# Optimization experiments

Hardware: AMD Instinct MI355X
Metric: run time of the kernel (lower is better)

Reference implementation:

```python
import jax, jax.numpy as jnp
import numpy as np

N_NODES = 50000
N_EDGES = 800000
IN_F, HID_F, OUT_F = 96, 96, 32


def setup_inputs() -> dict:
    key = jax.random.key(0)
    k1, k2, k3, k4, k5 = jax.random.split(key, 5)
    x = jax.random.normal(k1, (N_NODES, IN_F), dtype=jnp.float32)
    src = jax.random.randint(k2, (N_EDGES,), 0, N_NODES, dtype=jnp.int32)
    dst = jax.random.randint(k3, (N_EDGES,), 0, N_NODES, dtype=jnp.int32)
    W1 = jax.random.normal(k4, (IN_F, HID_F), dtype=jnp.float32) / np.sqrt(IN_F)
    b1 = jnp.zeros((HID_F,), dtype=jnp.float32)
    W2 = jax.random.normal(k5, (HID_F, OUT_F), dtype=jnp.float32) / np.sqrt(HID_F)
    b2 = jnp.zeros((OUT_F,), dtype=jnp.float32)
    return {"x": x, "src": src, "dst": dst, "W1": W1, "b1": b1, "W2": W2, "b2": b2}


def _graph_conv(src, dst, n_nodes, h, W, b):
    # DGL GraphConv, norm='both': D_out^{-1/2} A D_in^{-1/2} h W + b
    ones = jnp.ones((src.shape[0],), dtype=h.dtype)
    deg_out = jax.ops.segment_sum(ones, src, num_segments=n_nodes)  # src out-degree
    deg_in = jax.ops.segment_sum(ones, dst, num_segments=n_nodes)   # dst in-degree
    norm_src = jax.lax.rsqrt(jnp.maximum(deg_out, 1.0))
    norm_dst = jax.lax.rsqrt(jnp.maximum(deg_in, 1.0))
    h = h * norm_src[:, None]
    msg = h[src]                                                    # [E, F] gather
    agg = jax.ops.segment_sum(msg, dst, num_segments=n_nodes)       # [N, F] scatter-add
    agg = agg * norm_dst[:, None]
    return agg @ W + b


def reference(x, src, dst, W1, b1, W2, b2):
    n = x.shape[0]
    h = _graph_conv(src, dst, n, x, W1, b1)
    h = jax.nn.relu(h)
    h = _graph_conv(src, dst, n, h, W2, b2)
    return h
```

## Files before the change

kernel.cpp:

```cpp
#include <hip/hip_runtime.h>


constexpr int NN = 50000;
constexpr int NE = 800000;
constexpr int CAP = 64;
constexpr int HNODES = 16384;
constexpr int HWORDS = 8192;
constexpr int NCH = 4;
constexpr int NSL = 64;
constexpr int NNP = 50048;
constexpr int PREF_NB = (NN + 255) / 256;
constexpr int CVTW_NB = 48;
constexpr int FILL_NB = NCH * NSL;
constexpr int CVTX_NB = ((NN + 1) * 12 + 255) / 256;

using bf16x8 = __attribute__((ext_vector_type(8))) short;
using u16x8  = __attribute__((ext_vector_type(8))) unsigned short;
using f32x4  = __attribute__((ext_vector_type(4))) float;

__device__ __forceinline__ ushort f2b(float f) {
    unsigned u = __float_as_uint(f);
    u += 0x7FFFu + ((u >> 16) & 1u);
    return (ushort)(u >> 16);
}
__device__ __forceinline__ float b2f(ushort h) {
    return __uint_as_float(((unsigned)h) << 16);
}

__global__ void hist_kernel(const int* __restrict__ src, const int* __restrict__ dst,
                            ushort* __restrict__ pS, ushort* __restrict__ pD, int ne) {
    __shared__ int bins[HWORDS];
    const int ch = blockIdx.x, sl = blockIdx.y;
    const int lo = ch * HNODES;
    for (int i = threadIdx.x; i < HWORDS; i += 256) bins[i] = 0;
    __syncthreads();
    const int per4 = (ne / NSL) / 4;
    const int i0 = sl * per4;
    const int4* src4 = (const int4*)src;
    const int4* dst4 = (const int4*)dst;
    for (int i = i0 + threadIdx.x; i < i0 + per4; i += 256) {
        int4 s = src4[i];
        int4 d = dst4[i];
        unsigned u;
        u = (unsigned)(s.x - lo); if (u < HNODES) atomicAdd(bins + (u >> 1), 1 << ((u & 1) * 16));
        u = (unsigned)(s.y - lo); if (u < HNODES) atomicAdd(bins + (u >> 1), 1 << ((u & 1) * 16));
        u = (unsigned)(s.z - lo); if (u < HNODES) atomicAdd(bins + (u >> 1), 1 << ((u & 1) * 16));
        u = (unsigned)(s.w - lo); if (u < HNODES) atomicAdd(bins + (u >> 1), 1 << ((u & 1) * 16));
        u = (unsigned)(d.x - lo); if (u < HNODES) atomicAdd(bins + (u >> 1), 1 << ((u & 1) * 16 + 8));
        u = (unsigned)(d.y - lo); if (u < HNODES) atomicAdd(bins + (u >> 1), 1 << ((u & 1) * 16 + 8));
        u = (unsigned)(d.z - lo); if (u < HNODES) atomicAdd(bins + (u >> 1), 1 << ((u & 1) * 16 + 8));
        u = (unsigned)(d.w - lo); if (u < HNODES) atomicAdd(bins + (u >> 1), 1 << ((u & 1) * 16 + 8));
    }
    __syncthreads();
    for (int pi = threadIdx.x; pi < HWORDS; pi += 256) {
        int node = lo + 2 * pi;
        if (node >= NN) break;
        int w = bins[pi];
        unsigned sE = w & 0xFF, dE = (w >> 8) & 0xFF, sO = (w >> 16) & 0xFF, dO = (w >> 24) & 0xFF;
        if (node + 1 < NN) {
            *(unsigned*)&pS[(size_t)sl * NNP + node] = sE | (sO << 16);
            *(unsigned*)&pD[(size_t)sl * NNP + node] = dE | (dO << 16);
        } else {
            pS[(size_t)sl * NNP + node] = (ushort)sE;
            pD[(size_t)sl * NNP + node] = (ushort)dE;
        }
    }
}

__global__ void prefix_cvtw_kernel(const ushort* __restrict__ pS, ushort* __restrict__ pD,
                                   float* __restrict__ ns, int* __restrict__ cnt,
                                   const float* __restrict__ W1, const float* __restrict__ W2,
                                   ushort* __restrict__ W1t, ushort* __restrict__ W2t, int n) {
    int b = blockIdx.x;
    if (b < PREF_NB) {
        int i = b * 256 + threadIdx.x;
        if (i >= n) return;
        int sS = 0, run = 0;
#pragma unroll
        for (int sl = 0; sl < NSL; ++sl) {
            sS += pS[(size_t)sl * NNP + i];
            int c = pD[(size_t)sl * NNP + i];
            pD[(size_t)sl * NNP + i] = (ushort)run;
            run += c;
        }
        ns[i] = rsqrtf(fmaxf((float)sS, 1.0f));
        cnt[i] = run;
    } else {
        int i = (b - PREF_NB) * 256 + threadIdx.x;
        if (i < 96 * 96) {
            int k = i / 96, c = i % 96;
            W1t[c * 96 + k] = f2b(W1[i]);
        } else {
            int j = i - 96 * 96;
            int k = j / 32, c = j % 32;
            W2t[c * 96 + k] = f2b(W2[j]);
        }
    }
}

__global__ void fill_cvtx_kernel(const int* __restrict__ src, const int* __restrict__ dst,
                                 const ushort* __restrict__ pD, ushort* __restrict__ slots,
                                 const float* __restrict__ x, const float* __restrict__ ns,
                                 ushort* __restrict__ xh, int ne, int n) {
    __shared__ int cur[HWORDS];
    int b = blockIdx.x;
    if (b < FILL_NB) {
        const int ch = b / NSL, sl = b % NSL;
        const int lo = ch * HNODES;
        for (int pi = threadIdx.x; pi < HWORDS; pi += 256) {
            int node = lo + 2 * pi;
            int lov = (node < NN) ? (int)pD[(size_t)sl * NNP + node] : 0;
            int hiv = (node + 1 < NN) ? (int)pD[(size_t)sl * NNP + node + 1] : 0;
            cur[pi] = lov | (hiv << 16);
        }
        __syncthreads();
        const int per4 = (ne / NSL) / 4;
        const int i0 = sl * per4;
        const int4* src4 = (const int4*)src;
        const int4* dst4 = (const int4*)dst;
        for (int i = i0 + threadIdx.x; i < i0 + per4; i += 256) {
            int4 d = dst4[i];
            int4 s = src4[i];
            unsigned u; int sh, old, p;
            u = (unsigned)(d.x - lo);
            if (u < HNODES) { sh = (u & 1) * 16; old = atomicAdd(cur + (u >> 1), 1 << sh);
                p = (old >> sh) & 0xFFFF; if (p < CAP) slots[((size_t)(lo + u) << 6) + p] = (ushort)s.x; }
            u = (unsigned)(d.y - lo);
            if (u < HNODES) { sh = (u & 1) * 16; old = atomicAdd(cur + (u >> 1), 1 << sh);
                p = (old >> sh) & 0xFFFF; if (p < CAP) slots[((size_t)(lo + u) << 6) + p] = (ushort)s.y; }
            u = (unsigned)(d.z - lo);
            if (u < HNODES) { sh = (u & 1) * 16; old = atomicAdd(cur + (u >> 1), 1 << sh);
                p = (old >> sh) & 0xFFFF; if (p < CAP) slots[((size_t)(lo + u) << 6) + p] = (ushort)s.z; }
            u = (unsigned)(d.w - lo);
            if (u < HNODES) { sh = (u & 1) * 16; old = atomicAdd(cur + (u >> 1), 1 << sh);
                p = (old >> sh) & 0xFFFF; if (p < CAP) slots[((size_t)(lo + u) << 6) + p] = (ushort)s.w; }
        }
    } else {
        int t = (b - FILL_NB) * 256 + threadIdx.x;
        if (t >= (n + 1) * 12) return;
        int r = t / 12;
        u16x8 o;
        if (r == n) {
#pragma unroll
            for (int u = 0; u < 8; ++u) o[u] = 0;
        } else {
            float s = ns[r];
            const float4* p = (const float4*)(x) + (size_t)t * 2;
            float4 v0 = p[0], v1 = p[1];
            o[0] = f2b(s * v0.x); o[1] = f2b(s * v0.y); o[2] = f2b(s * v0.z); o[3] = f2b(s * v0.w);
            o[4] = f2b(s * v1.x); o[5] = f2b(s * v1.y); o[6] = f2b(s * v1.z); o[7] = f2b(s * v1.w);
        }
        *(u16x8*)&xh[(size_t)t * 8] = o;
    }
}

__global__ void agg1_kernel(const ushort* __restrict__ xh, const int* __restrict__ cnt,
                            const ushort* __restrict__ slots, ushort* __restrict__ AB, int n) {
    int tid = blockIdx.x * 256 + threadIdx.x;
    int r = tid / 12, q = tid % 12;
    if (r >= n) return;
    int deg = min(cnt[r], CAP);
    const ushort* br = slots + ((size_t)r << 6);
    float acc[8] = {};
    for (int j0 = 0; j0 < deg; j0 += 8) {
        u16x8 sl8 = *(const u16x8*)(br + j0);
        int s0 = (j0 + 0 < deg) ? (int)sl8[0] : n;
        int s1 = (j0 + 1 < deg) ? (int)sl8[1] : n;
        int s2 = (j0 + 2 < deg) ? (int)sl8[2] : n;
        int s3 = (j0 + 3 < deg) ? (int)sl8[3] : n;
        int s4 = (j0 + 4 < deg) ? (int)sl8[4] : n;
        int s5 = (j0 + 5 < deg) ? (int)sl8[5] : n;
        int s6 = (j0 + 6 < deg) ? (int)sl8[6] : n;
        int s7 = (j0 + 7 < deg) ? (int)sl8[7] : n;
        u16x8 v0 = *(const u16x8*)&xh[(size_t)s0 * 96 + q * 8];
        u16x8 v1 = *(const u16x8*)&xh[(size_t)s1 * 96 + q * 8];
        u16x8 v2 = *(const u16x8*)&xh[(size_t)s2 * 96 + q * 8];
        u16x8 v3 = *(const u16x8*)&xh[(size_t)s3 * 96 + q * 8];
        u16x8 v4 = *(const u16x8*)&xh[(size_t)s4 * 96 + q * 8];
        u16x8 v5 = *(const u16x8*)&xh[(size_t)s5 * 96 + q * 8];
        u16x8 v6 = *(const u16x8*)&xh[(size_t)s6 * 96 + q * 8];
        u16x8 v7 = *(const u16x8*)&xh[(size_t)s7 * 96 + q * 8];
#pragma unroll
        for (int t = 0; t < 8; ++t) acc[t] += b2f(v0[t]);
#pragma unroll
        for (int t = 0; t < 8; ++t) acc[t] += b2f(v1[t]);
#pragma unroll
        for (int t = 0; t < 8; ++t) acc[t] += b2f(v2[t]);
#pragma unroll
        for (int t = 0; t < 8; ++t) acc[t] += b2f(v3[t]);
#pragma unroll
        for (int t = 0; t < 8; ++t) acc[t] += b2f(v4[t]);
#pragma unroll
        for (int t = 0; t < 8; ++t) acc[t] += b2f(v5[t]);
#pragma unroll
        for (int t = 0; t < 8; ++t) acc[t] += b2f(v6[t]);
#pragma unroll
        for (int t = 0; t < 8; ++t) acc[t] += b2f(v7[t]);
    }
    u16x8 o;
#pragma unroll
    for (int t = 0; t < 8; ++t) o[t] = f2b(acc[t]);
    *(u16x8*)&AB[(size_t)r * 96 + q * 8] = o;
}

__global__ void __launch_bounds__(256) gemm12_fused(
        const ushort* __restrict__ AB, const ushort* __restrict__ W1t,
        const ushort* __restrict__ W2t, const float* __restrict__ b1,
        const float* __restrict__ ns, const int* __restrict__ cnt,
        ushort* __restrict__ t2h, int n) {
    __shared__ ushort Wl1[96 * 104];
    __shared__ ushort Wl2[32 * 104];
    __shared__ ushort Hl[64 * 104];
    for (int i = threadIdx.x; i < 1152; i += 256) {
        int nr = i / 12, k = (i % 12) * 8;
        *(bf16x8*)&Wl1[nr * 104 + k] = *(const bf16x8*)&W1t[nr * 96 + k];
    }
    for (int i = threadIdx.x; i < 384; i += 256) {
        int nr = i / 12, k = (i % 12) * 8;
        *(bf16x8*)&Wl2[nr * 104 + k] = *(const bf16x8*)&W2t[nr * 96 + k];
    }
    __syncthreads();

    const int lane = threadIdx.x & 63;
    const int w = threadIdx.x >> 6;
    const int rl = lane & 15, kg = lane >> 4;
    const int rowbase = blockIdx.x * 64 + w * 16;

    const ushort* arow = AB + (size_t)(rowbase + rl) * 96 + kg * 8;
    bf16x8 a0 = *(const bf16x8*)(arow);
    bf16x8 a1 = *(const bf16x8*)(arow + 32);
    bf16x8 a2 = *(const bf16x8*)(arow + 64);
    f32x4 acc1[6] = {};
#pragma unroll
    for (int nt = 0; nt < 6; ++nt) {
        const ushort* wr = &Wl1[(nt * 16 + rl) * 104 + kg * 8];
        acc1[nt] = __builtin_amdgcn_mfma_f32_16x16x32_bf16(a0, *(const bf16x8*)(wr),      acc1[nt], 0, 0, 0);
        acc1[nt] = __builtin_amdgcn_mfma_f32_16x16x32_bf16(a1, *(const bf16x8*)(wr + 32), acc1[nt], 0, 0, 0);
        acc1[nt] = __builtin_amdgcn_mfma_f32_16x16x32_bf16(a2, *(const bf16x8*)(wr + 64), acc1[nt], 0, 0, 0);
    }
    const int r0 = rowbase + kg * 4;
    float sj[4];
#pragma unroll
    for (int j = 0; j < 4; ++j) sj[j] = rsqrtf(fmaxf((float)cnt[r0 + j], 1.0f));
#pragma unroll
    for (int nt = 0; nt < 6; ++nt) {
        int col = nt * 16 + rl;
        float bc = b1[col];
#pragma unroll
        for (int j = 0; j < 4; ++j)
            Hl[(w * 16 + kg * 4 + j) * 104 + col] = f2b(fmaxf(acc1[nt][j] * sj[j] + bc, 0.f));
    }
    __syncthreads();

    const ushort* hrow = &Hl[(w * 16 + rl) * 104 + kg * 8];
    bf16x8 h0 = *(const bf16x8*)(hrow);
    bf16x8 h1 = *(const bf16x8*)(hrow + 32);
    bf16x8 h2 = *(const bf16x8*)(hrow + 64);
    f32x4 acc2[2] = {};
#pragma unroll
    for (int nt = 0; nt < 2; ++nt) {
        const ushort* wr = &Wl2[(nt * 16 + rl) * 104 + kg * 8];
        acc2[nt] = __builtin_amdgcn_mfma_f32_16x16x32_bf16(h0, *(const bf16x8*)(wr),      acc2[nt], 0, 0, 0);
        acc2[nt] = __builtin_amdgcn_mfma_f32_16x16x32_bf16(h1, *(const bf16x8*)(wr + 32), acc2[nt], 0, 0, 0);
        acc2[nt] = __builtin_amdgcn_mfma_f32_16x16x32_bf16(h2, *(const bf16x8*)(wr + 64), acc2[nt], 0, 0, 0);
    }
    float sn[4];
#pragma unroll
    for (int j = 0; j < 4; ++j) sn[j] = ns[r0 + j];
#pragma unroll
    for (int nt = 0; nt < 2; ++nt) {
        int col = nt * 16 + rl;
#pragma unroll
        for (int j = 0; j < 4; ++j) {
            float val = (r0 + j < n) ? acc2[nt][j] * sn[j] : 0.f;
            t2h[(size_t)(r0 + j) * 32 + col] = f2b(val);
        }
    }
}

__global__ void agg2_kernel(const ushort* __restrict__ t2h, const float* __restrict__ b2,
                            const int* __restrict__ cnt, const ushort* __restrict__ slots,
                            float* __restrict__ out, int n) {
    int tid = blockIdx.x * 256 + threadIdx.x;
    int r = tid / 4, q = tid % 4;
    if (r >= n) return;
    int deg = min(cnt[r], CAP);
    const ushort* br = slots + ((size_t)r << 6);
    float acc[8] = {};
    for (int j0 = 0; j0 < deg; j0 += 8) {
        u16x8 sl8 = *(const u16x8*)(br + j0);
        int s0 = (j0 + 0 < deg) ? (int)sl8[0] : n;
        int s1 = (j0 + 1 < deg) ? (int)sl8[1] : n;
        int s2 = (j0 + 2 < deg) ? (int)sl8[2] : n;
        int s3 = (j0 + 3 < deg) ? (int)sl8[3] : n;
        int s4 = (j0 + 4 < deg) ? (int)sl8[4] : n;
        int s5 = (j0 + 5 < deg) ? (int)sl8[5] : n;
        int s6 = (j0 + 6 < deg) ? (int)sl8[6] : n;
        int s7 = (j0 + 7 < deg) ? (int)sl8[7] : n;
        u16x8 v0 = *(const u16x8*)&t2h[(size_t)s0 * 32 + q * 8];
        u16x8 v1 = *(const u16x8*)&t2h[(size_t)s1 * 32 + q * 8];
        u16x8 v2 = *(const u16x8*)&t2h[(size_t)s2 * 32 + q * 8];
        u16x8 v3 = *(const u16x8*)&t2h[(size_t)s3 * 32 + q * 8];
        u16x8 v4 = *(const u16x8*)&t2h[(size_t)s4 * 32 + q * 8];
        u16x8 v5 = *(const u16x8*)&t2h[(size_t)s5 * 32 + q * 8];
        u16x8 v6 = *(const u16x8*)&t2h[(size_t)s6 * 32 + q * 8];
        u16x8 v7 = *(const u16x8*)&t2h[(size_t)s7 * 32 + q * 8];
#pragma unroll
        for (int t = 0; t < 8; ++t) acc[t] += b2f(v0[t]);
#pragma unroll
        for (int t = 0; t < 8; ++t) acc[t] += b2f(v1[t]);
#pragma unroll
        for (int t = 0; t < 8; ++t) acc[t] += b2f(v2[t]);
#pragma unroll
        for (int t = 0; t < 8; ++t) acc[t] += b2f(v3[t]);
#pragma unroll
        for (int t = 0; t < 8; ++t) acc[t] += b2f(v4[t]);
#pragma unroll
        for (int t = 0; t < 8; ++t) acc[t] += b2f(v5[t]);
#pragma unroll
        for (int t = 0; t < 8; ++t) acc[t] += b2f(v6[t]);
#pragma unroll
        for (int t = 0; t < 8; ++t) acc[t] += b2f(v7[t]);
    }
    float sd = rsqrtf(fmaxf((float)deg, 1.0f));
    const float4* bb = (const float4*)(b2 + q * 8);
    float4 bv0 = bb[0], bv1 = bb[1];
    float4 o0, o1;
    o0.x = acc[0] * sd + bv0.x; o0.y = acc[1] * sd + bv0.y;
    o0.z = acc[2] * sd + bv0.z; o0.w = acc[3] * sd + bv0.w;
    o1.x = acc[4] * sd + bv1.x; o1.y = acc[5] * sd + bv1.y;
    o1.z = acc[6] * sd + bv1.z; o1.w = acc[7] * sd + bv1.w;
    float4* po = (float4*)&out[(size_t)r * 32 + q * 8];
    po[0] = o0; po[1] = o1;
}

extern "C" void kernel_launch(void* const* d_in, const int* in_sizes, int n_in,
                              void* d_out, int out_size, void* d_ws, size_t ws_size,
                              hipStream_t stream) {
    const float* x   = (const float*)d_in[0];
    const int*   src = (const int*)d_in[1];
    const int*   dst = (const int*)d_in[2];
    const float* W1  = (const float*)d_in[3];
    const float* b1  = (const float*)d_in[4];
    const float* W2  = (const float*)d_in[5];
    const float* b2  = (const float*)d_in[6];
    float* out = (float*)d_out;

    int*    cnt   = (int*)d_ws;
    float*  ns    = (float*)(cnt + NNP);
    ushort* slots = (ushort*)(ns + NNP);
    ushort* pS    = slots + (size_t)NN * CAP;
    ushort* pD    = pS + (size_t)NSL * NNP;
    ushort* xh    = pD + (size_t)NSL * NNP;
    ushort* AB    = xh + (size_t)NNP * 96;
    ushort* t2h   = AB + (size_t)NNP * 96;
    ushort* W1t   = t2h + (size_t)NNP * 32;
    ushort* W2t   = W1t + 96 * 96;

    hist_kernel<<<dim3(NCH, NSL), 256, 0, stream>>>(src, dst, pS, pD, NE);
    prefix_cvtw_kernel<<<PREF_NB + CVTW_NB, 256, 0, stream>>>(pS, pD, ns, cnt, W1, W2, W1t, W2t, NN);
    fill_cvtx_kernel<<<FILL_NB + CVTX_NB, 256, 0, stream>>>(src, dst, pD, slots, x, ns, xh, NE, NN);

    agg1_kernel<<<(NN * 12 + 255) / 256, 256, 0, stream>>>(xh, cnt, slots, AB, NN);
    gemm12_fused<<<NNP / 64, 256, 0, stream>>>(AB, W1t, W2t, b1, ns, cnt, t2h, NN);
    agg2_kernel<<<(NN * 4 + 255) / 256, 256, 0, stream>>>(t2h, b2, cnt, slots, out, NN);
}
```

Baseline: 92.70 us.

## Pack degree histograms as 8-bit counters and halve node chunks

Per-slice degree histograms and prefix offsets now use one byte per node, four nodes per shared-memory word, instead of 16-bit fields. This lets each block cover about 25k nodes, so the number of node chunks drops from four to two. As a result each edge slice is read half as often in the histogram and fill kernels, and the pS/pD arrays shrink by half. The trade-off is more shared memory per histogram block, which may lower occupancy, and it relies on per-slice counts and per-node in-degree prefixes fitting in 8 bits.

```diff
diff --git a/kernel.cpp b/kernel.cpp
--- a/kernel.cpp
+++ b/kernel.cpp
@@ -4,11 +4,11 @@
 constexpr int NN = 50000;
 constexpr int NE = 800000;
 constexpr int CAP = 64;
-constexpr int HNODES = 16384;
-constexpr int HWORDS = 8192;
-constexpr int NCH = 4;
+constexpr int NNP = 50048;
+constexpr int HN  = 25024;
+constexpr int HW  = HN / 4;
+constexpr int NCH = 2;
 constexpr int NSL = 64;
-constexpr int NNP = 50048;
 constexpr int PREF_NB = (NN + 255) / 256;
 constexpr int CVTW_NB = 48;
 constexpr int FILL_NB = NCH * NSL;
@@ -28,11 +28,13 @@
 }
 
 __global__ void hist_kernel(const int* __restrict__ src, const int* __restrict__ dst,
-                            ushort* __restrict__ pS, ushort* __restrict__ pD, int ne) {
-    __shared__ int bins[HWORDS];
+                            unsigned char* __restrict__ pS, unsigned char* __restrict__ pD,
+                            int ne) {
+    __shared__ int binsS[HW];
+    __shared__ int binsD[HW];
     const int ch = blockIdx.x, sl = blockIdx.y;
-    const int lo = ch * HNODES;
-    for (int i = threadIdx.x; i < HWORDS; i += 256) bins[i] = 0;
+    const int lo = ch * HN;
+    for (int i = threadIdx.x; i < HW; i += 256) { binsS[i] = 0; binsD[i] = 0; }
     __syncthreads();
     const int per4 = (ne / NSL) / 4;
     const int i0 = sl * per4;
@@ -42,32 +44,26 @@
         int4 s = src4[i];
         int4 d = dst4[i];
         unsigned u;
-        u = (unsigned)(s.x - lo); if (u < HNODES) atomicAdd(bins + (u >> 1), 1 << ((u & 1) * 16));
-        u = (unsigned)(s.y - lo); if (u < HNODES) atomicAdd(bins + (u >> 1), 1 << ((u & 1) * 16));
-        u = (unsigned)(s.z - lo); if (u < HNODES) atomicAdd(bins + (u >> 1), 1 << ((u & 1) * 16));
-        u = (unsigned)(s.w - lo); if (u < HNODES) atomicAdd(bins + (u >> 1), 1 << ((u & 1) * 16));
-        u = (unsigned)(d.x - lo); if (u < HNODES) atomicAdd(bins + (u >> 1), 1 << ((u & 1) * 16 + 8));
-        u = (unsigned)(d.y - lo); if (u < HNODES) atomicAdd(bins + (u >> 1), 1 << ((u & 1) * 16 + 8));
-        u = (unsigned)(d.z - lo); if (u < HNODES) atomicAdd(bins + (u >> 1), 1 << ((u & 1) * 16 + 8));
-        u = (unsigned)(d.w - lo); if (u < HNODES) atomicAdd(bins + (u >> 1), 1 << ((u & 1) * 16 + 8));
+        u = (unsigned)(s.x - lo); if (u < HN) atomicAdd(binsS + (u >> 2), 1 << ((u & 3) * 8));
+        u = (unsigned)(s.y - lo); if (u < HN) atomicAdd(binsS + (u >> 2), 1 << ((u & 3) * 8));
+        u = (unsigned)(s.z - lo); if (u < HN) atomicAdd(binsS + (u >> 2), 1 << ((u & 3) * 8));
+        u = (unsigned)(s.w - lo); if (u < HN) atomicAdd(binsS + (u >> 2), 1 << ((u & 3) * 8));
+        u = (unsigned)(d.x - lo); if (u < HN) atomicAdd(binsD + (u >> 2), 1 << ((u & 3) * 8));
+        u = (unsigned)(d.y - lo); if (u < HN) atomicAdd(binsD + (u >> 2), 1 << ((u & 3) * 8));
+        u = (unsigned)(d.z - lo); if (u < HN) atomicAdd(binsD + (u >> 2), 1 << ((u & 3) * 8));
+        u = (unsigned)(d.w - lo); if (u < HN) atomicAdd(binsD + (u >> 2), 1 << ((u & 3) * 8));
     }
     __syncthreads();
-    for (int pi = threadIdx.x; pi < HWORDS; pi += 256) {
-        int node = lo + 2 * pi;
-        if (node >= NN) break;
-        int w = bins[pi];
-        unsigned sE = w & 0xFF, dE = (w >> 8) & 0xFF, sO = (w >> 16) & 0xFF, dO = (w >> 24) & 0xFF;
-        if (node + 1 < NN) {
-            *(unsigned*)&pS[(size_t)sl * NNP + node] = sE | (sO << 16);
-            *(unsigned*)&pD[(size_t)sl * NNP + node] = dE | (dO << 16);
-        } else {
-            pS[(size_t)sl * NNP + node] = (ushort)sE;
-            pD[(size_t)sl * NNP + node] = (ushort)dE;
-        }
-    }
-}
-
-__global__ void prefix_cvtw_kernel(const ushort* __restrict__ pS, ushort* __restrict__ pD,
+    int* oS = (int*)(pS + (size_t)sl * NNP + lo);
+    int* oD = (int*)(pD + (size_t)sl * NNP + lo);
+    for (int t = threadIdx.x; t < HW; t += 256) {
+        oS[t] = binsS[t];
+        oD[t] = binsD[t];
+    }
+}
+
+__global__ void prefix_cvtw_kernel(const unsigned char* __restrict__ pS,
+                                   unsigned char* __restrict__ pD,
                                    float* __restrict__ ns, int* __restrict__ cnt,
                                    const float* __restrict__ W1, const float* __restrict__ W2,
                                    ushort* __restrict__ W1t, ushort* __restrict__ W2t, int n) {
@@ -80,7 +76,7 @@
         for (int sl = 0; sl < NSL; ++sl) {
             sS += pS[(size_t)sl * NNP + i];
             int c = pD[(size_t)sl * NNP + i];
-            pD[(size_t)sl * NNP + i] = (ushort)run;
+            pD[(size_t)sl * NNP + i] = (unsigned char)run;
             run += c;
         }
         ns[i] = rsqrtf(fmaxf((float)sS, 1.0f));
@@ -99,20 +95,17 @@
 }
 
 __global__ void fill_cvtx_kernel(const int* __restrict__ src, const int* __restrict__ dst,
-                                 const ushort* __restrict__ pD, ushort* __restrict__ slots,
+                                 const unsigned char* __restrict__ pD,
+                                 ushort* __restrict__ slots,
                                  const float* __restrict__ x, const float* __restrict__ ns,
                                  ushort* __restrict__ xh, int ne, int n) {
-    __shared__ int cur[HWORDS];
+    __shared__ int cur[HW];
     int b = blockIdx.x;
     if (b < FILL_NB) {
-        const int ch = b / NSL, sl = b % NSL;
-        const int lo = ch * HNODES;
-        for (int pi = threadIdx.x; pi < HWORDS; pi += 256) {
-            int node = lo + 2 * pi;
-            int lov = (node < NN) ? (int)pD[(size_t)sl * NNP + node] : 0;
-            int hiv = (node + 1 < NN) ? (int)pD[(size_t)sl * NNP + node + 1] : 0;
-            cur[pi] = lov | (hiv << 16);
-        }
+        const int ch = b >> 6, sl = b & 63;
+        const int lo = ch * HN;
+        const int* ip = (const int*)(pD + (size_t)sl * NNP + lo);
+        for (int t = threadIdx.x; t < HW; t += 256) cur[t] = ip[t];
         __syncthreads();
         const int per4 = (ne / NSL) / 4;
         const int i0 = sl * per4;
@@ -123,17 +116,17 @@
             int4 s = src4[i];
             unsigned u; int sh, old, p;
             u = (unsigned)(d.x - lo);
-            if (u < HNODES) { sh = (u & 1) * 16; old = atomicAdd(cur + (u >> 1), 1 << sh);
-                p = (old >> sh) & 0xFFFF; if (p < CAP) slots[((size_t)(lo + u) << 6) + p] = (ushort)s.x; }
+            if (u < HN) { sh = (u & 3) * 8; old = atomicAdd(cur + (u >> 2), 1 << sh);
+                p = (old >> sh) & 0xFF; if (p < CAP) slots[((size_t)(lo + u) << 6) + p] = (ushort)s.x; }
             u = (unsigned)(d.y - lo);
-            if (u < HNODES) { sh = (u & 1) * 16; old = atomicAdd(cur + (u >> 1), 1 << sh);
-                p = (old >> sh) & 0xFFFF; if (p < CAP) slots[((size_t)(lo + u) << 6) + p] = (ushort)s.y; }
+            if (u < HN) { sh = (u & 3) * 8; old = atomicAdd(cur + (u >> 2), 1 << sh);
+                p = (old >> sh) & 0xFF; if (p < CAP) slots[((size_t)(lo + u) << 6) + p] = (ushort)s.y; }
             u = (unsigned)(d.z - lo);
-            if (u < HNODES) { sh = (u & 1) * 16; old = atomicAdd(cur + (u >> 1), 1 << sh);
-                p = (old >> sh) & 0xFFFF; if (p < CAP) slots[((size_t)(lo + u) << 6) + p] = (ushort)s.z; }
+            if (u < HN) { sh = (u & 3) * 8; old = atomicAdd(cur + (u >> 2), 1 << sh);
+                p = (old >> sh) & 0xFF; if (p < CAP) slots[((size_t)(lo + u) << 6) + p] = (ushort)s.z; }
             u = (unsigned)(d.w - lo);
-            if (u < HNODES) { sh = (u & 1) * 16; old = atomicAdd(cur + (u >> 1), 1 << sh);
-                p = (old >> sh) & 0xFFFF; if (p < CAP) slots[((size_t)(lo + u) << 6) + p] = (ushort)s.w; }
+            if (u < HN) { sh = (u & 3) * 8; old = atomicAdd(cur + (u >> 2), 1 << sh);
+                p = (old >> sh) & 0xFF; if (p < CAP) slots[((size_t)(lo + u) << 6) + p] = (ushort)s.w; }
         }
     } else {
         int t = (b - FILL_NB) * 256 + threadIdx.x;
@@ -349,9 +342,9 @@
     int*    cnt   = (int*)d_ws;
     float*  ns    = (float*)(cnt + NNP);
     ushort* slots = (ushort*)(ns + NNP);
-    ushort* pS    = slots + (size_t)NN * CAP;
-    ushort* pD    = pS + (size_t)NSL * NNP;
-    ushort* xh    = pD + (size_t)NSL * NNP;
+    unsigned char* pS = (unsigned char*)(slots + (size_t)NN * CAP);
+    unsigned char* pD = pS + (size_t)NSL * NNP;
+    ushort* xh    = (ushort*)(pD + (size_t)NSL * NNP);
     ushort* AB    = xh + (size_t)NNP * 96;
     ushort* t2h   = AB + (size_t)NNP * 96;
     ushort* W1t   = t2h + (size_t)NNP * 32;
```

After: 83.19 us. 1.11x faster.
